# Performance work log

Hardware: AMD Instinct MI355X
Metric: run time of the kernel (lower is better)

The kernel has to match this reference:

```python
import jax, jax.numpy as jnp
import numpy as np

B, S, D, H, AD, E = 4, 2048, 1024, 2048, 128, 8

def _ln(x, g, b, eps=1e-5):
    m = jnp.mean(x, axis=-1, keepdims=True)
    v = jnp.var(x, axis=-1, keepdims=True)
    return (x - m) * jax.lax.rsqrt(v + eps) * g + b

def setup_inputs() -> dict:
    key = jax.random.key(0)
    ks = jax.random.split(key, 12)
    scale = 1.0 / D ** 0.5
    ascale = scale * 0.01
    ead = 0.01 / AD ** 0.5
    return {
        'x': jax.random.normal(ks[0], (B, S, D), jnp.float32),
        'expert_weights': jax.random.uniform(ks[1], (B, S, E), jnp.float32),
        'Wu': jax.random.normal(ks[2], (H, D), jnp.float32) * scale,
        'bu': jnp.zeros((H,), jnp.float32),
        'Wg': jax.random.normal(ks[3], (H, D), jnp.float32) * scale,
        'bg': jnp.zeros((H,), jnp.float32),
        'Wd': jax.random.normal(ks[4], (D, H), jnp.float32) * scale,
        'bd': jnp.zeros((D,), jnp.float32),
        'Wpre': jax.random.normal(ks[5], (AD, D), jnp.float32) * ascale,
        'bpre': jnp.zeros((AD,), jnp.float32),
        'Wpost': jax.random.normal(ks[6], (AD, H), jnp.float32) * ascale,
        'bpost': jnp.zeros((AD,), jnp.float32),
        'ln_g': jnp.ones((AD,), jnp.float32),
        'ln_b': jnp.zeros((AD,), jnp.float32),
        'Wap': jax.random.normal(ks[7], (H, AD), jnp.float32) * ascale,
        'A': jax.random.normal(ks[8], (E, AD, AD), jnp.float32) * ead,
        'eg': jnp.ones((E, AD), jnp.float32),
        'eb': jnp.zeros((E, AD), jnp.float32),
        'Wp': jax.random.normal(ks[9], (H, AD), jnp.float32) * ead,
        'Wo': jax.random.normal(ks[10], (D, H), jnp.float32) * ead,
    }

def reference(x, expert_weights, Wu, bu, Wg, bg, Wd, bd, Wpre, bpre, Wpost, bpost, ln_g, ln_b, Wap, A, eg, eb, Wp, Wo):
    # ---- SharedExpertMLP ----
    up = x @ Wu.T + bu                      # [B,S,H]
    gate = x @ Wg.T + bg
    hidden = jax.nn.silu(gate) * up
    adapt_in = _ln(x @ Wpre.T + bpre, ln_g, ln_b)        # [B,S,AD]
    adapt_out = _ln(hidden @ Wpost.T + bpost, ln_g, ln_b)
    aw = jnp.einsum('bsa,bta->bst', adapt_in, adapt_out)  # [B,S,S]
    aw = jax.nn.silu(jnp.clip(aw, -5.0, 5.0))
    adapt = jnp.einsum('bst,bta->bsa', aw, adapt_in)
    hidden = hidden + 0.1 * (adapt @ Wap.T)
    shared = hidden @ Wd.T + bd                           # [B,S,D]
    # ---- expert branch (vectorized over experts) ----
    pre = x @ Wpre.T + bpre                               # [B,S,AD] (no adapt_norm here, as in torch)
    h = jnp.einsum('bsa,eca->ebsc', pre, A)               # per-expert adapter linear
    h = _ln(h, eg[:, None, None, :], eb[:, None, None, :])
    wmask = jnp.where(expert_weights > 0, expert_weights, 0.0)  # [B,S,E]
    hw = jnp.einsum('ebsa,bse->bsa', h, wmask)            # weighted combine before shared projections
    Wc = Wo @ Wp                                          # [D,AD]: output_proj(expert_proj(.))
    contrib = hw @ Wc.T                                   # [B,S,D]
    # sum_i w_i * (shared + 0.1*mask_i*expert_i) = shared*sum(w) + 0.1*sum(w_i*expert_i)
    return shared * jnp.sum(expert_weights, axis=-1, keepdims=True) + 0.1 * contrib
```

## Files before the change

kernel.cpp:

```cpp
#include <hip/hip_runtime.h>
#include <math.h>

#define BB 4
#define SS 2048
#define DD 1024
#define HH 2048
#define AD 128
#define EE 8
#define MM (BB*SS)

typedef unsigned short u16;
typedef short bf16x8 __attribute__((ext_vector_type(8)));
typedef float f32x4 __attribute__((ext_vector_type(4)));

__device__ __forceinline__ float silu_f(float x){ return x / (1.f + __expf(-x)); }

__device__ __forceinline__ u16 f2bf(float f){
    union { float f; unsigned u; } c; c.f = f;
    unsigned r = (c.u + 0x7FFFu + ((c.u >> 16) & 1u)) >> 16;
    return (u16)r;
}

__device__ __forceinline__ void gld16(const u16* g, u16* l){
    __builtin_amdgcn_global_load_lds((const __attribute__((address_space(1))) void*)g,
                                     (__attribute__((address_space(3))) void*)l, 16, 0, 0);
}

template<int EPI>
__global__ __launch_bounds__(256,2) void mfma_nt(
    const u16* __restrict__ A, const u16* __restrict__ B, void* Cv,
    int M, int N, int K, long sA, long sB, long sC)
{
    __shared__ __align__(16) u16 As[128*32];
    __shared__ __align__(16) u16 Bs[128*32];
    const int t = threadIdx.x;
    const int lane = t & 63;
    const int wv = t >> 6;
    const int m0 = blockIdx.y * 128, n0 = blockIdx.x * 128;
    const u16* Ab = A + (long)blockIdx.z * sA;
    const u16* Bb = B + (long)blockIdx.z * sB;
    const int srow = t >> 2, scol = (t & 3) * 8;
    const u16* ga0 = Ab + (long)(m0 + srow) * K + scol;
    const u16* ga1 = ga0 + 64L * K;
    const u16* gb0 = Bb + (long)(n0 + srow) * K + scol;
    const u16* gb1 = gb0 + 64L * K;
    u16* la0 = As + t * 8;  u16* la1 = As + 2048 + t * 8;
    u16* lb0 = Bs + t * 8;  u16* lb1 = Bs + 2048 + t * 8;
    const int fr = lane & 15, q = lane >> 4;
    const int wm = (wv & 1) * 64, wn = (wv >> 1) * 64;

    f32x4 acc[4][4] = {};
    for (int k0 = 0; k0 < K; k0 += 32) {
        gld16(ga0 + k0, la0);
        gld16(ga1 + k0, la1);
        gld16(gb0 + k0, lb0);
        gld16(gb1 + k0, lb1);
        __syncthreads();
        bf16x8 af[4], bfr[4];
        #pragma unroll
        for (int i = 0; i < 4; ++i) af[i]  = *(const bf16x8*)&As[(wm + i*16 + fr)*32 + q*8];
        #pragma unroll
        for (int i = 0; i < 4; ++i) bfr[i] = *(const bf16x8*)&Bs[(wn + i*16 + fr)*32 + q*8];
        #pragma unroll
        for (int mi = 0; mi < 4; ++mi)
            #pragma unroll
            for (int ni = 0; ni < 4; ++ni)
                acc[mi][ni] = __builtin_amdgcn_mfma_f32_16x16x32_bf16(af[mi], bfr[ni], acc[mi][ni], 0, 0, 0);
        __syncthreads();
    }

    u16* Cb = (u16*)Cv + (long)blockIdx.z * sC;
    #pragma unroll
    for (int mi = 0; mi < 4; ++mi)
        #pragma unroll
        for (int ni = 0; ni < 4; ++ni) {
            const int col = n0 + wn + ni*16 + fr;
            #pragma unroll
            for (int r = 0; r < 4; ++r) {
                const int row = m0 + wm + mi*16 + q*4 + r;
                float v = acc[mi][ni][r];
                v = fminf(fmaxf(v, -5.f), 5.f);
                Cb[(long)row * N + col] = f2bf(silu_f(v));
            }
        }
}

__global__ __launch_bounds__(256,2) void mfma_sk(
    const u16* __restrict__ A, const u16* __restrict__ B, float* __restrict__ P,
    int M, int K, int S, long sA, long sB, long sC, long sSplit)
{
    __shared__ __align__(16) u16 As[128*32];
    __shared__ __align__(16) u16 Bs[128*32];
    const int t = threadIdx.x;
    const int lane = t & 63;
    const int wv = t >> 6;
    const int s = blockIdx.x;
    const int m0 = blockIdx.y * 128;
    const u16* Ab = A + (long)blockIdx.z * sA;
    const u16* Bb = B + (long)blockIdx.z * sB;
    const int srow = t >> 2, scol = (t & 3) * 8;
    const int Ks = K / S, kBeg = s * Ks;
    const u16* ga0 = Ab + (long)(m0 + srow) * K + scol + kBeg;
    const u16* ga1 = ga0 + 64L * K;
    const u16* gb0 = Bb + (long)srow * K + scol + kBeg;
    const u16* gb1 = gb0 + 64L * K;
    u16* la0 = As + t * 8;  u16* la1 = As + 2048 + t * 8;
    u16* lb0 = Bs + t * 8;  u16* lb1 = Bs + 2048 + t * 8;
    const int fr = lane & 15, q = lane >> 4;
    const int wm = (wv & 1) * 64, wn = (wv >> 1) * 64;

    f32x4 acc[4][4] = {};
    for (int k0 = 0; k0 < Ks; k0 += 32) {
        gld16(ga0 + k0, la0);
        gld16(ga1 + k0, la1);
        gld16(gb0 + k0, lb0);
        gld16(gb1 + k0, lb1);
        __syncthreads();
        bf16x8 af[4], bfr[4];
        #pragma unroll
        for (int i = 0; i < 4; ++i) af[i]  = *(const bf16x8*)&As[(wm + i*16 + fr)*32 + q*8];
        #pragma unroll
        for (int i = 0; i < 4; ++i) bfr[i] = *(const bf16x8*)&Bs[(wn + i*16 + fr)*32 + q*8];
        #pragma unroll
        for (int mi = 0; mi < 4; ++mi)
            #pragma unroll
            for (int ni = 0; ni < 4; ++ni)
                acc[mi][ni] = __builtin_amdgcn_mfma_f32_16x16x32_bf16(af[mi], bfr[ni], acc[mi][ni], 0, 0, 0);
        __syncthreads();
    }

    float* Pf = P + (long)s * sSplit + (long)blockIdx.z * sC;
    #pragma unroll
    for (int mi = 0; mi < 4; ++mi)
        #pragma unroll
        for (int ni = 0; ni < 4; ++ni) {
            const int col = wn + ni*16 + fr;
            #pragma unroll
            for (int r = 0; r < 4; ++r) {
                const int row = m0 + wm + mi*16 + q*4 + r;
                Pf[(long)row * 128 + col] = acc[mi][ni][r];
            }
        }
}

__global__ __launch_bounds__(256,2) void mfma_upgate(
    const u16* __restrict__ X, const u16* __restrict__ Wu_, const u16* __restrict__ Wg_,
    const float* __restrict__ bu, const float* __restrict__ bg, u16* __restrict__ H)
{
    __shared__ __align__(16) u16 Xs[128*32];
    __shared__ __align__(16) u16 Us[128*32];
    __shared__ __align__(16) u16 Gs[128*32];
    const int t = threadIdx.x, lane = t & 63, wv = t >> 6;
    const int m0 = blockIdx.y * 128, n0 = blockIdx.x * 128;
    const int srow = t >> 2, scol = (t & 3) * 8;
    const u16* gx0 = X   + (long)(m0 + srow) * DD + scol;
    const u16* gx1 = gx0 + 64L * DD;
    const u16* gu0 = Wu_ + (long)(n0 + srow) * DD + scol;
    const u16* gu1 = gu0 + 64L * DD;
    const u16* gg0 = Wg_ + (long)(n0 + srow) * DD + scol;
    const u16* gg1 = gg0 + 64L * DD;
    const int fr = lane & 15, q = lane >> 4;
    const int wm = (wv & 1) * 64, wn = (wv >> 1) * 64;

    f32x4 accu[4][4] = {};
    f32x4 accg[4][4] = {};
    for (int k0 = 0; k0 < DD; k0 += 32) {
        gld16(gx0 + k0, Xs + t*8);
        gld16(gx1 + k0, Xs + 2048 + t*8);
        gld16(gu0 + k0, Us + t*8);
        gld16(gu1 + k0, Us + 2048 + t*8);
        gld16(gg0 + k0, Gs + t*8);
        gld16(gg1 + k0, Gs + 2048 + t*8);
        __syncthreads();
        bf16x8 xf[4], uf[4], gf[4];
        #pragma unroll
        for (int i = 0; i < 4; ++i) {
            xf[i] = *(const bf16x8*)&Xs[(wm + i*16 + fr)*32 + q*8];
            uf[i] = *(const bf16x8*)&Us[(wn + i*16 + fr)*32 + q*8];
            gf[i] = *(const bf16x8*)&Gs[(wn + i*16 + fr)*32 + q*8];
        }
        #pragma unroll
        for (int mi = 0; mi < 4; ++mi)
            #pragma unroll
            for (int ni = 0; ni < 4; ++ni) {
                accu[mi][ni] = __builtin_amdgcn_mfma_f32_16x16x32_bf16(xf[mi], uf[ni], accu[mi][ni], 0, 0, 0);
                accg[mi][ni] = __builtin_amdgcn_mfma_f32_16x16x32_bf16(xf[mi], gf[ni], accg[mi][ni], 0, 0, 0);
            }
        __syncthreads();
    }
    #pragma unroll
    for (int mi = 0; mi < 4; ++mi) {
        #pragma unroll
        for (int ni = 0; ni < 4; ++ni) {
            const int col = n0 + wn + ni*16 + fr;
            #pragma unroll
            for (int r = 0; r < 4; ++r) {
                const int row = m0 + wm + mi*16 + q*4 + r;
                const float u = accu[mi][ni][r] + bu[col];
                const float g = accg[mi][ni][r] + bg[col];
                H[(long)row * HH + col] = f2bf(silu_f(g) * u);
            }
        }
    }
}

__global__ __launch_bounds__(256,2) void mfma_final(
    const u16* __restrict__ Hh, const u16* __restrict__ Wd_,
    const u16* __restrict__ Ac, const u16* __restrict__ Wcat,
    const float* __restrict__ bd, const float* __restrict__ sumw,
    float* __restrict__ out)
{
    __shared__ __align__(16) u16 As[128*32];
    __shared__ __align__(16) u16 Bs[128*32];
    const int t = threadIdx.x, lane = t & 63, wv = t >> 6;
    const int m0 = blockIdx.y * 128, n0 = blockIdx.x * 128;
    const int srow = t >> 2, scol = (t & 3) * 8;
    const int fr = lane & 15, q = lane >> 4;
    const int wm = (wv & 1) * 64, wn = (wv >> 1) * 64;
    u16* la0 = As + t * 8;  u16* la1 = As + 2048 + t * 8;
    u16* lb0 = Bs + t * 8;  u16* lb1 = Bs + 2048 + t * 8;

    f32x4 acc[4][4] = {};
    {
        const u16* ga0 = Hh  + (long)(m0 + srow) * HH + scol;
        const u16* ga1 = ga0 + 64L * HH;
        const u16* gb0 = Wd_ + (long)(n0 + srow) * HH + scol;
        const u16* gb1 = gb0 + 64L * HH;
        for (int k0 = 0; k0 < HH; k0 += 32) {
            gld16(ga0 + k0, la0);
            gld16(ga1 + k0, la1);
            gld16(gb0 + k0, lb0);
            gld16(gb1 + k0, lb1);
            __syncthreads();
            bf16x8 af[4], bfr[4];
            #pragma unroll
            for (int i = 0; i < 4; ++i) af[i]  = *(const bf16x8*)&As[(wm + i*16 + fr)*32 + q*8];
            #pragma unroll
            for (int i = 0; i < 4; ++i) bfr[i] = *(const bf16x8*)&Bs[(wn + i*16 + fr)*32 + q*8];
            #pragma unroll
            for (int mi = 0; mi < 4; ++mi)
                #pragma unroll
                for (int ni = 0; ni < 4; ++ni)
                    acc[mi][ni] = __builtin_amdgcn_mfma_f32_16x16x32_bf16(af[mi], bfr[ni], acc[mi][ni], 0, 0, 0);
            __syncthreads();
        }
    }
    f32x4 acc2[4][4] = {};
    {
        const u16* ga0 = Ac   + (long)(m0 + srow) * 256 + scol;
        const u16* ga1 = ga0 + 64L * 256;
        const u16* gb0 = Wcat + (long)(n0 + srow) * 256 + scol;
        const u16* gb1 = gb0 + 64L * 256;
        for (int k0 = 0; k0 < 256; k0 += 32) {
            gld16(ga0 + k0, la0);
            gld16(ga1 + k0, la1);
            gld16(gb0 + k0, lb0);
            gld16(gb1 + k0, lb1);
            __syncthreads();
            bf16x8 af[4], bfr[4];
            #pragma unroll
            for (int i = 0; i < 4; ++i) af[i]  = *(const bf16x8*)&As[(wm + i*16 + fr)*32 + q*8];
            #pragma unroll
            for (int i = 0; i < 4; ++i) bfr[i] = *(const bf16x8*)&Bs[(wn + i*16 + fr)*32 + q*8];
            #pragma unroll
            for (int mi = 0; mi < 4; ++mi)
                #pragma unroll
                for (int ni = 0; ni < 4; ++ni)
                    acc2[mi][ni] = __builtin_amdgcn_mfma_f32_16x16x32_bf16(af[mi], bfr[ni], acc2[mi][ni], 0, 0, 0);
            __syncthreads();
        }
    }
    #pragma unroll
    for (int mi = 0; mi < 4; ++mi)
        #pragma unroll
        for (int ni = 0; ni < 4; ++ni) {
            const int col = n0 + wn + ni*16 + fr;
            #pragma unroll
            for (int r = 0; r < 4; ++r) {
                const int row = m0 + wm + mi*16 + q*4 + r;
                out[(long)row * DD + col] =
                    sumw[row] * (acc[mi][ni][r] + bd[col]) + 0.1f * acc2[mi][ni][r];
            }
        }
}

__global__ __launch_bounds__(256) void expert_fused(
    const u16* __restrict__ pre, const u16* __restrict__ aexp,
    const float* __restrict__ ew, const float* __restrict__ eg,
    const float* __restrict__ eb, u16* __restrict__ acat,
    float* __restrict__ sumw)
{
    __shared__ float ewsh[64*8];
    __shared__ float egsh[8*128], ebsh[8*128];
    const int t = threadIdx.x, lane = t & 63, wv = t >> 6;
    const int fr = lane & 15, q = lane >> 4;
    const int wm = wv * 16;
    const int m0 = blockIdx.x * 64;
    if (t < 128) {
        const int row = t >> 1, j = (t & 1)*4;
        *(float4*)&ewsh[row*8+j] = *(const float4*)&ew[(long)(m0+row)*EE + j];
    }
    {   const int e = t >> 5, c = (t & 31)*4;
        *(float4*)&egsh[e*128+c] = *(const float4*)&eg[e*128+c];
        *(float4*)&ebsh[e*128+c] = *(const float4*)&eb[e*128+c]; }
    __syncthreads();

    f32x4 hwacc[8] = {};
    for (int e = 0; e < EE; ++e) {
        f32x4 acc[8] = {};
        const u16* Ae = aexp + (long)e * AD * AD;
        #pragma unroll
        for (int ks = 0; ks < 4; ++ks) {
            bf16x8 af, bfr[8];
            af = *(const bf16x8*)&pre[(long)(m0 + wm + fr)*AD + ks*32 + q*8];
            #pragma unroll
            for (int ni = 0; ni < 8; ++ni)
                bfr[ni] = *(const bf16x8*)&Ae[(long)(ni*16 + fr)*AD + ks*32 + q*8];
            #pragma unroll
            for (int ni = 0; ni < 8; ++ni)
                acc[ni] = __builtin_amdgcn_mfma_f32_16x16x32_bf16(af, bfr[ni], acc[ni], 0, 0, 0);
        }
        #pragma unroll
        for (int r = 0; r < 4; ++r) {
            float s = 0.f, s2 = 0.f;
            #pragma unroll
            for (int ni = 0; ni < 8; ++ni) { const float v = acc[ni][r]; s += v; s2 += v*v; }
            #pragma unroll
            for (int msk = 1; msk < 16; msk <<= 1) {
                s  += __shfl_xor(s,  msk, 64);
                s2 += __shfl_xor(s2, msk, 64);
            }
            const float mean = s * (1.f/128.f);
            const float var  = s2 * (1.f/128.f) - mean*mean;
            const float rs   = rsqrtf(var + 1e-5f);
            const int rowl = wm + q*4 + r;
            float w = ewsh[rowl*8 + e]; w = w > 0.f ? w : 0.f;
            #pragma unroll
            for (int ni = 0; ni < 8; ++ni) {
                const int col = ni*16 + fr;
                hwacc[ni][r] += w * ((acc[ni][r] - mean) * rs * egsh[e*128+col] + ebsh[e*128+col]);
            }
        }
    }
    #pragma unroll
    for (int r = 0; r < 4; ++r) {
        const int rowl = wm + q*4 + r;
        #pragma unroll
        for (int ni = 0; ni < 8; ++ni)
            acat[(long)(m0+rowl)*256 + ni*16 + fr] = f2bf(hwacc[ni][r]);
        if (fr == 0) {
            float sw = 0.f;
            #pragma unroll
            for (int j = 0; j < 8; ++j) sw += ewsh[rowl*8 + j];
            sumw[m0 + rowl] = sw;
        }
    }
}

template<int S>
__global__ __launch_bounds__(128) void ln_reduce(
    const float* __restrict__ P, long sSplit, const float* __restrict__ bias,
    u16* __restrict__ raw, u16* __restrict__ ln_out,
    const float* __restrict__ g, const float* __restrict__ b)
{
    const int r = blockIdx.x, tid = threadIdx.x;
    float v = bias[tid];
    #pragma unroll
    for (int s = 0; s < S; ++s) v += P[(long)s * sSplit + (long)r * AD + tid];
    if (raw) raw[(long)r * AD + tid] = f2bf(v);
    __shared__ float red[AD], red2[AD];
    red[tid] = v; red2[tid] = v*v;
    __syncthreads();
    for (int s = 64; s > 0; s >>= 1) {
        if (tid < s) { red[tid] += red[tid+s]; red2[tid] += red2[tid+s]; }
        __syncthreads();
    }
    const float mean = red[0] * (1.f/AD);
    const float var  = red2[0] * (1.f/AD) - mean*mean;
    const float rs   = rsqrtf(var + 1e-5f);
    ln_out[(long)r * AD + tid] = f2bf((v - mean) * rs * g[tid] + b[tid]);
}

__global__ __launch_bounds__(256) void reduce_cat(
    const float* __restrict__ P, u16* __restrict__ Wcat)
{
    const int i = blockIdx.x * 256 + threadIdx.x;
    const int a4 = i & 31, z = (i >> 5) & 1, d = i >> 6;
    const float* src = P + (long)z * (4L*DD*AD) + (long)d * AD + a4*4;
    float4 v = *(const float4*)src;
    #pragma unroll
    for (int s = 1; s < 4; ++s) {
        const float4 w = *(const float4*)(src + (long)s * DD * AD);
        v.x += w.x; v.y += w.y; v.z += w.z; v.w += w.w;
    }
    ushort4 o; o.x=f2bf(v.x); o.y=f2bf(v.y); o.z=f2bf(v.z); o.w=f2bf(v.w);
    ((ushort4*)Wcat)[(long)d*64 + z*32 + a4] = o;
}

__global__ __launch_bounds__(256) void reduce_adapt(
    const float* __restrict__ P, const float* __restrict__ sumw, u16* __restrict__ acat)
{
    const int i = blockIdx.x * 256 + threadIdx.x;
    const int perz = SS*AD/4;
    const int z = i / perz, local = i - z * perz;
    const float4* base = (const float4*)P + (long)z * 2 * perz;
    float4 v = base[local];
    const float4 w2 = base[local + perz];
    v.x += w2.x; v.y += w2.y; v.z += w2.z; v.w += w2.w;
    const long grow = i >> 5;
    const float sw = sumw[grow];
    ushort4 o;
    o.x = f2bf(sw*v.x); o.y = f2bf(sw*v.y); o.z = f2bf(sw*v.z); o.w = f2bf(sw*v.w);
    ((ushort4*)acat)[grow*64 + 32 + (i & 31)] = o;
}

__global__ __launch_bounds__(256) void transpose_bf(
    const u16* __restrict__ in, u16* __restrict__ out, long sIn, long sOut)
{
    __shared__ u16 tile[32][33];
    in  += (long)blockIdx.z * sIn;
    out += (long)blockIdx.z * sOut;
    const int x0 = blockIdx.x * 32, y0 = blockIdx.y * 32;
    const int tx = threadIdx.x & 31, ty = threadIdx.x >> 5;
    #pragma unroll
    for (int j = 0; j < 4; ++j)
        tile[ty + j*8][tx] = in[(long)(y0 + ty + j*8) * AD + x0 + tx];
    __syncthreads();
    #pragma unroll
    for (int j = 0; j < 4; ++j)
        out[(long)(x0 + ty + j*8) * SS + y0 + tx] = tile[tx][ty + j*8];
}

struct Cvt5 { const float* in[5]; u16* out[5]; long cum[6]; };
__global__ __launch_bounds__(256) void cvt_pack(Cvt5 a)
{
    const long i = (long)blockIdx.x * 256 + threadIdx.x;
    if (i >= a.cum[5]) return;
    int s = 0;
    while (i >= a.cum[s+1]) ++s;
    const long j = i - a.cum[s];
    const float4 v = ((const float4*)a.in[s])[j];
    ushort4 o;
    o.x = f2bf(v.x); o.y = f2bf(v.y); o.z = f2bf(v.z); o.w = f2bf(v.w);
    ((ushort4*)a.out[s])[j] = o;
}

extern "C" void kernel_launch(void* const* d_in, const int* in_sizes, int n_in,
                              void* d_out, int out_size, void* d_ws, size_t ws_size,
                              hipStream_t stream) {
    const float* x    = (const float*)d_in[0];
    const float* ew   = (const float*)d_in[1];
    const float* Wu   = (const float*)d_in[2];
    const float* bu   = (const float*)d_in[3];
    const float* Wg   = (const float*)d_in[4];
    const float* bg   = (const float*)d_in[5];
    const float* Wd   = (const float*)d_in[6];
    const float* bd   = (const float*)d_in[7];
    const float* Wpre = (const float*)d_in[8];
    const float* bpre = (const float*)d_in[9];
    const float* Wpost= (const float*)d_in[10];
    const float* bpost= (const float*)d_in[11];
    const float* ln_g = (const float*)d_in[12];
    const float* ln_b = (const float*)d_in[13];
    const float* Wap  = (const float*)d_in[14];
    const float* Aex  = (const float*)d_in[15];
    const float* eg   = (const float*)d_in[16];
    const float* eb   = (const float*)d_in[17];
    const float* Wp   = (const float*)d_in[18];
    const float* Wo   = (const float*)d_in[19];
    float* out = (float*)d_out;

    char* p = (char*)d_ws;
    auto take = [&](long bytes) -> char* {
        char* r = p; p += (bytes + 255) & ~255L; return r;
    };
    u16* x_slot  = (u16*)take(16777216);
    u16* wslot   = (u16*)take((long)2*DD*HH*2);
    u16* wpre    = (u16*)take((long)AD*DD*2);
    u16* aex     = (u16*)take((long)EE*AD*AD*2);
    u16* pre_bf  = (u16*)take((long)MM*AD*2);
    u16* ai_bf   = (u16*)take((long)MM*AD*2);
    char* shareA = take(33554432);
    u16* acat    = (u16*)take((long)MM*256*2);
    float* sumw  = (float*)take((long)MM*4);
    u16* hidden  = (u16*)take((long)MM*HH*2);

    u16* x_bf    = x_slot;
    u16* aiT     = x_slot;
    u16* wRaw    = aiT  + 1048576;
    u16* wT      = wRaw + 524288;
    u16* wpost_w = wT   + 524288;
    u16* wcat    = wpost_w + 262144;
    u16* ao_bf   = wcat + 262144;
    float* wcP   = (float*)(ao_bf + 1048576);
    float* awaiP = (float*)wcP;
    float* preP   = (float*)shareA;
    float* wpostP = (float*)shareA;
    u16*   aw     = (u16*)shareA;

    {
        Cvt5 a;
        a.in[0]=x;    a.out[0]=x_bf;              long n0=(long)MM*DD/4;
        a.in[1]=Wu;   a.out[1]=wslot;             long n1=(long)HH*DD/4;
        a.in[2]=Wg;   a.out[2]=wslot+(long)DD*HH; long n2=(long)HH*DD/4;
        a.in[3]=Wpre; a.out[3]=wpre;              long n3=(long)AD*DD/4;
        a.in[4]=Aex;  a.out[4]=aex;               long n4=(long)EE*AD*AD/4;
        a.cum[0]=0; a.cum[1]=n0; a.cum[2]=n0+n1; a.cum[3]=n0+n1+n2;
        a.cum[4]=n0+n1+n2+n3; a.cum[5]=n0+n1+n2+n3+n4;
        cvt_pack<<<dim3((a.cum[5]+255)/256), 256, 0, stream>>>(a);
    }
    mfma_sk<<<dim3(4, MM/128, 1), 256, 0, stream>>>(
        x_bf, wpre, preP, MM, DD, 4, 0, 0, 0, (long)MM*AD);
    ln_reduce<4><<<dim3(MM), 128, 0, stream>>>(preP, (long)MM*AD, bpre, pre_bf, ai_bf, ln_g, ln_b);
    expert_fused<<<dim3(MM/64), 256, 0, stream>>>(pre_bf, aex, ew, eg, eb, acat, sumw);
    mfma_upgate<<<dim3(HH/128, MM/128, 1), 256, 0, stream>>>(
        x_bf, wslot, wslot+(long)DD*HH, bu, bg, hidden);
    {
        Cvt5 a;
        a.in[0]=Wo;    a.out[0]=wslot;             long n0=(long)DD*HH/4;
        a.in[1]=Wd;    a.out[1]=wslot+(long)DD*HH; long n1=(long)DD*HH/4;
        a.in[2]=Wpost; a.out[2]=wpost_w;           long n2=(long)AD*HH/4;
        a.in[3]=Wp;    a.out[3]=wRaw;              long n3=(long)HH*AD/4;
        a.in[4]=Wap;   a.out[4]=wRaw+(long)HH*AD;  long n4=(long)HH*AD/4;
        a.cum[0]=0; a.cum[1]=n0; a.cum[2]=n0+n1; a.cum[3]=n0+n1+n2;
        a.cum[4]=n0+n1+n2+n3; a.cum[5]=n0+n1+n2+n3+n4;
        cvt_pack<<<dim3((a.cum[5]+255)/256), 256, 0, stream>>>(a);
    }
    transpose_bf<<<dim3(4,64,2), 256, 0, stream>>>(wRaw, wT, (long)HH*AD, (long)AD*HH);
    mfma_sk<<<dim3(4, DD/128, 2), 256, 0, stream>>>(
        wslot, wT, wcP, DD, HH, 4, (long)DD*HH, (long)AD*HH, 4L*DD*AD, (long)DD*AD);
    reduce_cat<<<dim3(256), 256, 0, stream>>>(wcP, wcat);
    mfma_sk<<<dim3(8, MM/128, 1), 256, 0, stream>>>(
        hidden, wpost_w, wpostP, MM, HH, 8, 0, 0, 0, (long)MM*AD);
    ln_reduce<8><<<dim3(MM), 128, 0, stream>>>(wpostP, (long)MM*AD, bpost, nullptr, ao_bf, ln_g, ln_b);
    transpose_bf<<<dim3(4,64,4), 256, 0, stream>>>(ai_bf, aiT, (long)SS*AD, (long)AD*SS);
    mfma_nt<2><<<dim3(SS/128, SS/128, BB), 256, 0, stream>>>(ai_bf, ao_bf, aw,
        SS, SS, AD, (long)SS*AD, (long)SS*AD, (long)SS*SS);
    mfma_sk<<<dim3(2, SS/128, BB), 256, 0, stream>>>(
        aw, aiT, awaiP, SS, SS, 2, (long)SS*SS, (long)AD*SS, 2L*SS*AD, (long)SS*AD);
    reduce_adapt<<<dim3((long)MM*AD/4/256), 256, 0, stream>>>(awaiP, sumw, acat);
    mfma_final<<<dim3(DD/128, MM/128), 256, 0, stream>>>(
        hidden, wslot+(long)DD*HH, acat, wcat, bd, sumw, out);
}
```

Measured before the change: 439.5 us.

## Fuse adapter attention into flash-style kernel and switch GEMMs to 32x32 MFMA

```diff
diff --git a/kernel.cpp b/kernel.cpp
--- a/kernel.cpp
+++ b/kernel.cpp
@@ -8,10 +8,12 @@
 #define AD 128
 #define EE 8
 #define MM (BB*SS)
+#define PS 136
 
 typedef unsigned short u16;
 typedef short bf16x8 __attribute__((ext_vector_type(8)));
 typedef float f32x4 __attribute__((ext_vector_type(4)));
+typedef float f32x16 __attribute__((ext_vector_type(16)));
 
 __device__ __forceinline__ float silu_f(float x){ return x / (1.f + __expf(-x)); }
 
@@ -24,65 +26,6 @@
 __device__ __forceinline__ void gld16(const u16* g, u16* l){
     __builtin_amdgcn_global_load_lds((const __attribute__((address_space(1))) void*)g,
                                      (__attribute__((address_space(3))) void*)l, 16, 0, 0);
-}
-
-template<int EPI>
-__global__ __launch_bounds__(256,2) void mfma_nt(
-    const u16* __restrict__ A, const u16* __restrict__ B, void* Cv,
-    int M, int N, int K, long sA, long sB, long sC)
-{
-    __shared__ __align__(16) u16 As[128*32];
-    __shared__ __align__(16) u16 Bs[128*32];
-    const int t = threadIdx.x;
-    const int lane = t & 63;
-    const int wv = t >> 6;
-    const int m0 = blockIdx.y * 128, n0 = blockIdx.x * 128;
-    const u16* Ab = A + (long)blockIdx.z * sA;
-    const u16* Bb = B + (long)blockIdx.z * sB;
-    const int srow = t >> 2, scol = (t & 3) * 8;
-    const u16* ga0 = Ab + (long)(m0 + srow) * K + scol;
-    const u16* ga1 = ga0 + 64L * K;
-    const u16* gb0 = Bb + (long)(n0 + srow) * K + scol;
-    const u16* gb1 = gb0 + 64L * K;
-    u16* la0 = As + t * 8;  u16* la1 = As + 2048 + t * 8;
-    u16* lb0 = Bs + t * 8;  u16* lb1 = Bs + 2048 + t * 8;
-    const int fr = lane & 15, q = lane >> 4;
-    const int wm = (wv & 1) * 64, wn = (wv >> 1) * 64;
-
-    f32x4 acc[4][4] = {};
-    for (int k0 = 0; k0 < K; k0 += 32) {
-        gld16(ga0 + k0, la0);
-        gld16(ga1 + k0, la1);
-        gld16(gb0 + k0, lb0);
-        gld16(gb1 + k0, lb1);
-        __syncthreads();
-        bf16x8 af[4], bfr[4];
-        #pragma unroll
-        for (int i = 0; i < 4; ++i) af[i]  = *(const bf16x8*)&As[(wm + i*16 + fr)*32 + q*8];
-        #pragma unroll
-        for (int i = 0; i < 4; ++i) bfr[i] = *(const bf16x8*)&Bs[(wn + i*16 + fr)*32 + q*8];
-        #pragma unroll
-        for (int mi = 0; mi < 4; ++mi)
-            #pragma unroll
-            for (int ni = 0; ni < 4; ++ni)
-                acc[mi][ni] = __builtin_amdgcn_mfma_f32_16x16x32_bf16(af[mi], bfr[ni], acc[mi][ni], 0, 0, 0);
-        __syncthreads();
-    }
-
-    u16* Cb = (u16*)Cv + (long)blockIdx.z * sC;
-    #pragma unroll
-    for (int mi = 0; mi < 4; ++mi)
-        #pragma unroll
-        for (int ni = 0; ni < 4; ++ni) {
-            const int col = n0 + wn + ni*16 + fr;
-            #pragma unroll
-            for (int r = 0; r < 4; ++r) {
-                const int row = m0 + wm + mi*16 + q*4 + r;
-                float v = acc[mi][ni][r];
-                v = fminf(fmaxf(v, -5.f), 5.f);
-                Cb[(long)row * N + col] = f2bf(silu_f(v));
-            }
-        }
 }
 
 __global__ __launch_bounds__(256,2) void mfma_sk(
@@ -159,11 +102,11 @@
     const u16* gu1 = gu0 + 64L * DD;
     const u16* gg0 = Wg_ + (long)(n0 + srow) * DD + scol;
     const u16* gg1 = gg0 + 64L * DD;
-    const int fr = lane & 15, q = lane >> 4;
+    const int l31 = lane & 31, kh = lane >> 5;
     const int wm = (wv & 1) * 64, wn = (wv >> 1) * 64;
 
-    f32x4 accu[4][4] = {};
-    f32x4 accg[4][4] = {};
+    f32x16 accu[2][2] = {};
+    f32x16 accg[2][2] = {};
     for (int k0 = 0; k0 < DD; k0 += 32) {
         gld16(gx0 + k0, Xs + t*8);
         gld16(gx1 + k0, Xs + 2048 + t*8);
@@ -172,36 +115,39 @@
         gld16(gg0 + k0, Gs + t*8);
         gld16(gg1 + k0, Gs + 2048 + t*8);
         __syncthreads();
-        bf16x8 xf[4], uf[4], gf[4];
-        #pragma unroll
-        for (int i = 0; i < 4; ++i) {
-            xf[i] = *(const bf16x8*)&Xs[(wm + i*16 + fr)*32 + q*8];
-            uf[i] = *(const bf16x8*)&Us[(wn + i*16 + fr)*32 + q*8];
-            gf[i] = *(const bf16x8*)&Gs[(wn + i*16 + fr)*32 + q*8];
-        }
-        #pragma unroll
-        for (int mi = 0; mi < 4; ++mi)
-            #pragma unroll
-            for (int ni = 0; ni < 4; ++ni) {
-                accu[mi][ni] = __builtin_amdgcn_mfma_f32_16x16x32_bf16(xf[mi], uf[ni], accu[mi][ni], 0, 0, 0);
-                accg[mi][ni] = __builtin_amdgcn_mfma_f32_16x16x32_bf16(xf[mi], gf[ni], accg[mi][ni], 0, 0, 0);
-            }
+        bf16x8 xf[2][2], uf[2][2], gf[2][2];
+        #pragma unroll
+        for (int mt = 0; mt < 2; ++mt)
+            #pragma unroll
+            for (int ks = 0; ks < 2; ++ks) {
+                xf[mt][ks] = *(const bf16x8*)&Xs[(wm + mt*32 + l31)*32 + ks*16 + kh*8];
+                uf[mt][ks] = *(const bf16x8*)&Us[(wn + mt*32 + l31)*32 + ks*16 + kh*8];
+                gf[mt][ks] = *(const bf16x8*)&Gs[(wn + mt*32 + l31)*32 + ks*16 + kh*8];
+            }
+        #pragma unroll
+        for (int mt = 0; mt < 2; ++mt)
+            #pragma unroll
+            for (int nt = 0; nt < 2; ++nt)
+                #pragma unroll
+                for (int ks = 0; ks < 2; ++ks) {
+                    accu[mt][nt] = __builtin_amdgcn_mfma_f32_32x32x16_bf16(xf[mt][ks], uf[nt][ks], accu[mt][nt], 0, 0, 0);
+                    accg[mt][nt] = __builtin_amdgcn_mfma_f32_32x32x16_bf16(xf[mt][ks], gf[nt][ks], accg[mt][nt], 0, 0, 0);
+                }
         __syncthreads();
     }
     #pragma unroll
-    for (int mi = 0; mi < 4; ++mi) {
-        #pragma unroll
-        for (int ni = 0; ni < 4; ++ni) {
-            const int col = n0 + wn + ni*16 + fr;
-            #pragma unroll
-            for (int r = 0; r < 4; ++r) {
-                const int row = m0 + wm + mi*16 + q*4 + r;
-                const float u = accu[mi][ni][r] + bu[col];
-                const float g = accg[mi][ni][r] + bg[col];
+    for (int mt = 0; mt < 2; ++mt)
+        #pragma unroll
+        for (int nt = 0; nt < 2; ++nt) {
+            const int col = n0 + wn + nt*32 + l31;
+            #pragma unroll
+            for (int r = 0; r < 16; ++r) {
+                const int row = m0 + wm + mt*32 + (r & 3) + 8*(r >> 2) + 4*kh;
+                const float u = accu[mt][nt][r] + bu[col];
+                const float g = accg[mt][nt][r] + bg[col];
                 H[(long)row * HH + col] = f2bf(silu_f(g) * u);
             }
         }
-    }
 }
 
 __global__ __launch_bounds__(256,2) void mfma_final(
@@ -215,12 +161,12 @@
     const int t = threadIdx.x, lane = t & 63, wv = t >> 6;
     const int m0 = blockIdx.y * 128, n0 = blockIdx.x * 128;
     const int srow = t >> 2, scol = (t & 3) * 8;
-    const int fr = lane & 15, q = lane >> 4;
+    const int l31 = lane & 31, kh = lane >> 5;
     const int wm = (wv & 1) * 64, wn = (wv >> 1) * 64;
     u16* la0 = As + t * 8;  u16* la1 = As + 2048 + t * 8;
     u16* lb0 = Bs + t * 8;  u16* lb1 = Bs + 2048 + t * 8;
 
-    f32x4 acc[4][4] = {};
+    f32x16 acc[2][2] = {};
     {
         const u16* ga0 = Hh  + (long)(m0 + srow) * HH + scol;
         const u16* ga1 = ga0 + 64L * HH;
@@ -232,20 +178,25 @@
             gld16(gb0 + k0, lb0);
             gld16(gb1 + k0, lb1);
             __syncthreads();
-            bf16x8 af[4], bfr[4];
-            #pragma unroll
-            for (int i = 0; i < 4; ++i) af[i]  = *(const bf16x8*)&As[(wm + i*16 + fr)*32 + q*8];
-            #pragma unroll
-            for (int i = 0; i < 4; ++i) bfr[i] = *(const bf16x8*)&Bs[(wn + i*16 + fr)*32 + q*8];
-            #pragma unroll
-            for (int mi = 0; mi < 4; ++mi)
-                #pragma unroll
-                for (int ni = 0; ni < 4; ++ni)
-                    acc[mi][ni] = __builtin_amdgcn_mfma_f32_16x16x32_bf16(af[mi], bfr[ni], acc[mi][ni], 0, 0, 0);
+            bf16x8 af[2][2], bf[2][2];
+            #pragma unroll
+            for (int mt = 0; mt < 2; ++mt)
+                #pragma unroll
+                for (int ks = 0; ks < 2; ++ks) {
+                    af[mt][ks] = *(const bf16x8*)&As[(wm + mt*32 + l31)*32 + ks*16 + kh*8];
+                    bf[mt][ks] = *(const bf16x8*)&Bs[(wn + mt*32 + l31)*32 + ks*16 + kh*8];
+                }
+            #pragma unroll
+            for (int mt = 0; mt < 2; ++mt)
+                #pragma unroll
+                for (int nt = 0; nt < 2; ++nt)
+                    #pragma unroll
+                    for (int ks = 0; ks < 2; ++ks)
+                        acc[mt][nt] = __builtin_amdgcn_mfma_f32_32x32x16_bf16(af[mt][ks], bf[nt][ks], acc[mt][nt], 0, 0, 0);
             __syncthreads();
         }
     }
-    f32x4 acc2[4][4] = {};
+    f32x16 acc2[2][2] = {};
     {
         const u16* ga0 = Ac   + (long)(m0 + srow) * 256 + scol;
         const u16* ga1 = ga0 + 64L * 256;
@@ -257,6 +208,70 @@
             gld16(gb0 + k0, lb0);
             gld16(gb1 + k0, lb1);
             __syncthreads();
+            bf16x8 af[2][2], bf[2][2];
+            #pragma unroll
+            for (int mt = 0; mt < 2; ++mt)
+                #pragma unroll
+                for (int ks = 0; ks < 2; ++ks) {
+                    af[mt][ks] = *(const bf16x8*)&As[(wm + mt*32 + l31)*32 + ks*16 + kh*8];
+                    bf[mt][ks] = *(const bf16x8*)&Bs[(wn + mt*32 + l31)*32 + ks*16 + kh*8];
+                }
+            #pragma unroll
+            for (int mt = 0; mt < 2; ++mt)
+                #pragma unroll
+                for (int nt = 0; nt < 2; ++nt)
+                    #pragma unroll
+                    for (int ks = 0; ks < 2; ++ks)
+                        acc2[mt][nt] = __builtin_amdgcn_mfma_f32_32x32x16_bf16(af[mt][ks], bf[nt][ks], acc2[mt][nt], 0, 0, 0);
+            __syncthreads();
+        }
+    }
+    #pragma unroll
+    for (int mt = 0; mt < 2; ++mt)
+        #pragma unroll
+        for (int nt = 0; nt < 2; ++nt) {
+            const int col = n0 + wn + nt*32 + l31;
+            #pragma unroll
+            for (int r = 0; r < 16; ++r) {
+                const int row = m0 + wm + mt*32 + (r & 3) + 8*(r >> 2) + 4*kh;
+                out[(long)row * DD + col] =
+                    sumw[row] * (acc[mt][nt][r] + bd[col]) + 0.1f * acc2[mt][nt][r];
+            }
+        }
+}
+
+__global__ __launch_bounds__(256,2) void flash_pv(
+    const u16* __restrict__ ai, const u16* __restrict__ ao,
+    const u16* __restrict__ aiT, float* __restrict__ adaptP)
+{
+    __shared__ __align__(16) u16 As[128*32];
+    __shared__ __align__(16) u16 Bs[128*32];
+    __shared__ __align__(16) u16 Psh[128*PS];
+    const int t = threadIdx.x, lane = t & 63, wv = t >> 6;
+    const int fr = lane & 15, q = lane >> 4;
+    const int wm = (wv & 1) * 64, wn = (wv >> 1) * 64;
+    const int tg = blockIdx.x, s0 = blockIdx.y * 128, b = blockIdx.z;
+    const u16* aib  = ai  + (long)b * SS * AD;
+    const u16* aob  = ao  + (long)b * SS * AD;
+    const u16* aiTb = aiT + (long)b * AD * SS;
+    const int srow = t >> 2, scol = (t & 3) * 8;
+    u16* la0 = As + t * 8;  u16* la1 = As + 2048 + t * 8;
+    u16* lb0 = Bs + t * 8;  u16* lb1 = Bs + 2048 + t * 8;
+    const u16* ga0 = aib + (long)(s0 + srow) * AD + scol;
+    const u16* ga1 = ga0 + 64L * AD;
+
+    f32x4 vacc[4][4] = {};
+    for (int ti = 0; ti < 2; ++ti) {
+        const int t0 = tg * 256 + ti * 128;
+        const u16* gb0 = aob + (long)(t0 + srow) * AD + scol;
+        const u16* gb1 = gb0 + 64L * AD;
+        f32x4 acc[4][4] = {};
+        for (int k0 = 0; k0 < AD; k0 += 32) {
+            gld16(ga0 + k0, la0);
+            gld16(ga1 + k0, la1);
+            gld16(gb0 + k0, lb0);
+            gld16(gb1 + k0, lb1);
+            __syncthreads();
             bf16x8 af[4], bfr[4];
             #pragma unroll
             for (int i = 0; i < 4; ++i) af[i]  = *(const bf16x8*)&As[(wm + i*16 + fr)*32 + q*8];
@@ -266,22 +281,65 @@
             for (int mi = 0; mi < 4; ++mi)
                 #pragma unroll
                 for (int ni = 0; ni < 4; ++ni)
-                    acc2[mi][ni] = __builtin_amdgcn_mfma_f32_16x16x32_bf16(af[mi], bfr[ni], acc2[mi][ni], 0, 0, 0);
+                    acc[mi][ni] = __builtin_amdgcn_mfma_f32_16x16x32_bf16(af[mi], bfr[ni], acc[mi][ni], 0, 0, 0);
             __syncthreads();
         }
-    }
+        #pragma unroll
+        for (int mi = 0; mi < 4; ++mi)
+            #pragma unroll
+            for (int ni = 0; ni < 4; ++ni)
+                #pragma unroll
+                for (int r = 0; r < 4; ++r) {
+                    float v = acc[mi][ni][r];
+                    v = fminf(fmaxf(v, -5.f), 5.f);
+                    Psh[(wm + mi*16 + q*4 + r)*PS + wn + ni*16 + fr] = f2bf(silu_f(v));
+                }
+        __syncthreads();
+        #pragma unroll
+        for (int kk = 0; kk < 4; ++kk) {
+            bf16x8 pf[4], bi[4];
+            #pragma unroll
+            for (int mi = 0; mi < 4; ++mi)
+                pf[mi] = *(const bf16x8*)&Psh[(wm + mi*16 + fr)*PS + kk*32 + q*8];
+            #pragma unroll
+            for (int ni = 0; ni < 4; ++ni)
+                bi[ni] = *(const bf16x8*)&aiTb[(long)(wn + ni*16 + fr)*SS + t0 + kk*32 + q*8];
+            #pragma unroll
+            for (int mi = 0; mi < 4; ++mi)
+                #pragma unroll
+                for (int ni = 0; ni < 4; ++ni)
+                    vacc[mi][ni] = __builtin_amdgcn_mfma_f32_16x16x32_bf16(pf[mi], bi[ni], vacc[mi][ni], 0, 0, 0);
+        }
+    }
+    float* Pf = adaptP + (long)tg * MM * AD + (long)(b * SS + s0) * AD;
     #pragma unroll
     for (int mi = 0; mi < 4; ++mi)
         #pragma unroll
         for (int ni = 0; ni < 4; ++ni) {
-            const int col = n0 + wn + ni*16 + fr;
+            const int col = wn + ni*16 + fr;
             #pragma unroll
             for (int r = 0; r < 4; ++r) {
-                const int row = m0 + wm + mi*16 + q*4 + r;
-                out[(long)row * DD + col] =
-                    sumw[row] * (acc[mi][ni][r] + bd[col]) + 0.1f * acc2[mi][ni][r];
-            }
-        }
+                const int row = wm + mi*16 + q*4 + r;
+                Pf[(long)row * AD + col] = vacc[mi][ni][r];
+            }
+        }
+}
+
+__global__ __launch_bounds__(256) void scale_adapt(
+    const float* __restrict__ P, const float* __restrict__ sumw, u16* __restrict__ acat)
+{
+    const int i = blockIdx.x * 256 + threadIdx.x;
+    float4 v = ((const float4*)P)[i];
+    #pragma unroll
+    for (int tg = 1; tg < 8; ++tg) {
+        const float4 w = ((const float4*)P)[i + (long)tg * (MM*AD/4)];
+        v.x += w.x; v.y += w.y; v.z += w.z; v.w += w.w;
+    }
+    const long grow = i >> 5;
+    const float sw = sumw[grow];
+    ushort4 o;
+    o.x = f2bf(sw*v.x); o.y = f2bf(sw*v.y); o.z = f2bf(sw*v.z); o.w = f2bf(sw*v.w);
+    ((ushort4*)acat)[grow*64 + 32 + (i & 31)] = o;
 }
 
 __global__ __launch_bounds__(256) void expert_fused(
@@ -397,29 +455,15 @@
     ((ushort4*)Wcat)[(long)d*64 + z*32 + a4] = o;
 }
 
-__global__ __launch_bounds__(256) void reduce_adapt(
-    const float* __restrict__ P, const float* __restrict__ sumw, u16* __restrict__ acat)
-{
-    const int i = blockIdx.x * 256 + threadIdx.x;
-    const int perz = SS*AD/4;
-    const int z = i / perz, local = i - z * perz;
-    const float4* base = (const float4*)P + (long)z * 2 * perz;
-    float4 v = base[local];
-    const float4 w2 = base[local + perz];
-    v.x += w2.x; v.y += w2.y; v.z += w2.z; v.w += w2.w;
-    const long grow = i >> 5;
-    const float sw = sumw[grow];
-    ushort4 o;
-    o.x = f2bf(sw*v.x); o.y = f2bf(sw*v.y); o.z = f2bf(sw*v.z); o.w = f2bf(sw*v.w);
-    ((ushort4*)acat)[grow*64 + 32 + (i & 31)] = o;
-}
-
-__global__ __launch_bounds__(256) void transpose_bf(
-    const u16* __restrict__ in, u16* __restrict__ out, long sIn, long sOut)
+__global__ __launch_bounds__(256) void transpose6(
+    const u16* __restrict__ wRaw, u16* __restrict__ wT,
+    const u16* __restrict__ ai, u16* __restrict__ aiT)
 {
     __shared__ u16 tile[32][33];
-    in  += (long)blockIdx.z * sIn;
-    out += (long)blockIdx.z * sOut;
+    const int z = blockIdx.z;
+    const u16* in; u16* out;
+    if (z < 2) { in = wRaw + (long)z * HH * AD; out = wT + (long)z * AD * HH; }
+    else       { in = ai + (long)(z-2) * SS * AD; out = aiT + (long)(z-2) * AD * SS; }
     const int x0 = blockIdx.x * 32, y0 = blockIdx.y * 32;
     const int tx = threadIdx.x & 31, ty = threadIdx.x >> 5;
     #pragma unroll
@@ -493,10 +537,9 @@
     u16* wcat    = wpost_w + 262144;
     u16* ao_bf   = wcat + 262144;
     float* wcP   = (float*)(ao_bf + 1048576);
-    float* awaiP = (float*)wcP;
     float* preP   = (float*)shareA;
     float* wpostP = (float*)shareA;
-    u16*   aw     = (u16*)shareA;
+    float* adaptP = (float*)shareA;
 
     {
         Cvt5 a;
@@ -526,19 +569,15 @@
         a.cum[4]=n0+n1+n2+n3; a.cum[5]=n0+n1+n2+n3+n4;
         cvt_pack<<<dim3((a.cum[5]+255)/256), 256, 0, stream>>>(a);
     }
-    transpose_bf<<<dim3(4,64,2), 256, 0, stream>>>(wRaw, wT, (long)HH*AD, (long)AD*HH);
+    transpose6<<<dim3(4,64,6), 256, 0, stream>>>(wRaw, wT, ai_bf, aiT);
     mfma_sk<<<dim3(4, DD/128, 2), 256, 0, stream>>>(
         wslot, wT, wcP, DD, HH, 4, (long)DD*HH, (long)AD*HH, 4L*DD*AD, (long)DD*AD);
     reduce_cat<<<dim3(256), 256, 0, stream>>>(wcP, wcat);
     mfma_sk<<<dim3(8, MM/128, 1), 256, 0, stream>>>(
         hidden, wpost_w, wpostP, MM, HH, 8, 0, 0, 0, (long)MM*AD);
     ln_reduce<8><<<dim3(MM), 128, 0, stream>>>(wpostP, (long)MM*AD, bpost, nullptr, ao_bf, ln_g, ln_b);
-    transpose_bf<<<dim3(4,64,4), 256, 0, stream>>>(ai_bf, aiT, (long)SS*AD, (long)AD*SS);
-    mfma_nt<2><<<dim3(SS/128, SS/128, BB), 256, 0, stream>>>(ai_bf, ao_bf, aw,
-        SS, SS, AD, (long)SS*AD, (long)SS*AD, (long)SS*SS);
-    mfma_sk<<<dim3(2, SS/128, BB), 256, 0, stream>>>(
-        aw, aiT, awaiP, SS, SS, 2, (long)SS*SS, (long)AD*SS, 2L*SS*AD, (long)SS*AD);
-    reduce_adapt<<<dim3((long)MM*AD/4/256), 256, 0, stream>>>(awaiP, sumw, acat);
+    flash_pv<<<dim3(8, SS/128, BB), 256, 0, stream>>>(ai_bf, ao_bf, aiT, adaptP);
+    scale_adapt<<<dim3((long)MM*AD/4/256), 256, 0, stream>>>(adaptP, sumw, acat);
     mfma_final<<<dim3(DD/128, MM/128), 256, 0, stream>>>(
         hidden, wslot+(long)DD*HH, acat, wcat, bd, sumw, out);
 }
```

Result: no change. 436.7 us (-0.7%).
